# Kernel optimization log

Hardware: AMD Instinct MI355X
Metric: run time of the kernel (lower is better)

The kernel has to match this reference:

```python
import jax, jax.numpy as jnp
import numpy as np

D = 1024
H = 16
FF = 4096
B = 2
L = 2048
EPS = 1e-5


def setup_inputs() -> dict:
    key = jax.random.key(0)
    ks = jax.random.split(key, 12)
    s = 0.02
    return {
        "x": jax.random.normal(ks[0], (B, L, D), dtype=jnp.float32),
        "ln1_g": jnp.ones((D,), jnp.float32),
        "ln1_b": jnp.zeros((D,), jnp.float32),
        "qkv_w": jax.random.normal(ks[1], (D, 3 * D), dtype=jnp.float32) * s,
        "proj_w": jax.random.normal(ks[2], (D, D), dtype=jnp.float32) * s,
        "proj_b": jnp.zeros((D,), jnp.float32),
        "ln2_g": jnp.ones((D,), jnp.float32),
        "ln2_b": jnp.zeros((D,), jnp.float32),
        "w1": jax.random.normal(ks[3], (D, FF), dtype=jnp.float32) * s,
        "b1": jnp.zeros((FF,), jnp.float32),
        "w2": jax.random.normal(ks[4], (FF, D), dtype=jnp.float32) * s,
        "b2": jnp.zeros((D,), jnp.float32),
    }


def _layernorm(x, g, b):
    mu = jnp.mean(x, axis=-1, keepdims=True)
    var = jnp.var(x, axis=-1, keepdims=True)
    return (x - mu) * jax.lax.rsqrt(var + EPS) * g + b


def _attn(x, qkv_w, proj_w, proj_b):
    Bv, Lv, Dv = x.shape
    dk = Dv // H
    qkv = x @ qkv_w  # [B,L,3D]
    q, k, v = jnp.split(qkv, 3, axis=-1)

    def split(t):
        return t.reshape(Bv, Lv, H, dk).transpose(0, 2, 1, 3)  # [B,H,L,dk]

    q, k, v = map(split, (q, k, v))
    scores = jnp.einsum("bhqd,bhkd->bhqk", q, k) / np.sqrt(dk)
    attn = jax.nn.softmax(scores, axis=-1)
    out = jnp.einsum("bhqk,bhkd->bhqd", attn, v)
    out = out.transpose(0, 2, 1, 3).reshape(Bv, Lv, Dv)
    return out @ proj_w + proj_b


def reference(x, ln1_g, ln1_b, qkv_w, proj_w, proj_b, ln2_g, ln2_b, w1, b1, w2, b2):
    x = x + _attn(_layernorm(x, ln1_g, ln1_b), qkv_w, proj_w, proj_b)
    h = _layernorm(x, ln2_g, ln2_b)
    h = jax.nn.gelu(h @ w1 + b1, approximate=False) @ w2 + b2
    return x + h
```

## Files before the change

### kernel.cpp

```cpp
#include <hip/hip_runtime.h>
#include <cstdint>
#include <cstddef>

typedef __attribute__((ext_vector_type(8))) short bf16x8;
typedef __attribute__((ext_vector_type(4))) short bf16x4;
typedef __attribute__((ext_vector_type(4))) float f32x4;

__device__ __forceinline__ uint16_t f2bf(float f) {
    uint32_t u = __float_as_uint(f);
    u += 0x7FFFu + ((u >> 16) & 1u);
    return (uint16_t)(u >> 16);
}
__device__ __forceinline__ uint32_t bfr(float f) {
    return (__float_as_uint(f) + 0x8000u) >> 16;
}

__device__ __forceinline__ f32x4 mfma16(bf16x8 a, bf16x8 b, f32x4 c) {
    return __builtin_amdgcn_mfma_f32_16x16x32_bf16(a, b, c, 0, 0, 0);
}

__device__ __forceinline__ void async_copy16(const void* g, void* l) {
    __builtin_amdgcn_global_load_lds(
        (__attribute__((address_space(1))) void*)g,
        (__attribute__((address_space(3))) void*)l, 16, 0, 0);
}

typedef __attribute__((address_space(3))) const uint16_t lds_cu16;
__device__ __forceinline__ bf16x4 tr_read(lds_cu16* p) {
    bf16x4 d;
    asm volatile("ds_read_b64_tr_b16 %0, %1" : "=v"(d) : "v"(p));
    return d;
}
__device__ __forceinline__ bf16x8 cat8(bf16x4 lo, bf16x4 hi) {
    return __builtin_shufflevector(lo, hi, 0, 1, 2, 3, 4, 5, 6, 7);
}

__global__ __launch_bounds__(256) void transpose_cast(const float* __restrict__ W,
                                                      uint16_t* __restrict__ Wt,
                                                      int K, int N) {
    __shared__ uint16_t tile[32][33];
    const int n0 = blockIdx.x * 32, k0 = blockIdx.y * 32;
    const int tx = threadIdx.x, ty = threadIdx.y;
#pragma unroll
    for (int j = 0; j < 4; ++j) {
        int k = k0 + ty + j * 8;
        tile[ty + j * 8][tx] = f2bf(W[(size_t)k * N + n0 + tx]);
    }
    __syncthreads();
#pragma unroll
    for (int j = 0; j < 4; ++j) {
        int n = n0 + ty + j * 8;
        Wt[(size_t)n * K + k0 + tx] = tile[tx][ty + j * 8];
    }
}

__global__ __launch_bounds__(256) void ln_kernel(const float* __restrict__ x,
                                                 const float* __restrict__ g,
                                                 const float* __restrict__ b,
                                                 uint16_t* __restrict__ out) {
    const int row = blockIdx.x;
    const int t = threadIdx.x;
    const float* xr = x + (size_t)row * 1024;
    float4 v = *(const float4*)(xr + t * 4);
    float s = v.x + v.y + v.z + v.w;
    float s2 = v.x * v.x + v.y * v.y + v.z * v.z + v.w * v.w;
#pragma unroll
    for (int off = 1; off < 64; off <<= 1) {
        s += __shfl_xor(s, off);
        s2 += __shfl_xor(s2, off);
    }
    __shared__ float sh[8];
    const int wv = t >> 6;
    if ((t & 63) == 0) { sh[wv] = s; sh[4 + wv] = s2; }
    __syncthreads();
    s = sh[0] + sh[1] + sh[2] + sh[3];
    s2 = sh[4] + sh[5] + sh[6] + sh[7];
    const float mu = s * (1.f / 1024.f);
    const float var = s2 * (1.f / 1024.f) - mu * mu;
    const float rs = rsqrtf(var + 1e-5f);
    float4 gg = *(const float4*)(g + t * 4);
    float4 bb = *(const float4*)(b + t * 4);
    ushort4 ov;
    ov.x = f2bf((v.x - mu) * rs * gg.x + bb.x);
    ov.y = f2bf((v.y - mu) * rs * gg.y + bb.y);
    ov.z = f2bf((v.z - mu) * rs * gg.z + bb.z);
    ov.w = f2bf((v.w - mu) * rs * gg.w + bb.w);
    *(ushort4*)(out + (size_t)row * 1024 + t * 4) = ov;
}

template <int EPI, int BM, int BN>
__global__ __launch_bounds__(256) void gemm_bt(const uint16_t* __restrict__ A,
                                               const uint16_t* __restrict__ Bt,
                                               const float* __restrict__ bias,
                                               const float* __restrict__ resid,
                                               void* __restrict__ outp,
                                               int M, int N, int K) {
    __shared__ uint16_t As[BM * 64];
    __shared__ uint16_t Bs[BN * 64];
    const int t = threadIdx.x, lane = t & 63, w = t >> 6;
    const int l16 = lane & 15, lhi = lane >> 4;
    const int wr = w >> 1, wc = w & 1;
    const int m0 = blockIdx.x * BM, n0 = blockIdx.y * BN;
    constexpr int MI = BM / 32, NI = BN / 32;

    f32x4 acc[MI][NI];
    const f32x4 z = {0.f, 0.f, 0.f, 0.f};
#pragma unroll
    for (int mi = 0; mi < MI; ++mi)
#pragma unroll
        for (int ni = 0; ni < NI; ++ni) acc[mi][ni] = z;

    const int srow = lane >> 3;
    const int sgs = ((lane & 7) ^ srow) << 3;
    const uint16_t* Abase = A + (size_t)m0 * K;
    const uint16_t* Bbase = Bt + (size_t)n0 * K;

    for (int kt = 0; kt < K; kt += 64) {
        __syncthreads();
#pragma unroll
        for (int p = 0; p < BM / 32; ++p) {
            int r0 = w * (BM / 4) + p * 8;
            async_copy16(Abase + (size_t)(r0 + srow) * K + kt + sgs, &As[r0 * 64]);
        }
#pragma unroll
        for (int p = 0; p < BN / 32; ++p) {
            int r0 = w * (BN / 4) + p * 8;
            async_copy16(Bbase + (size_t)(r0 + srow) * K + kt + sgs, &Bs[r0 * 64]);
        }
        __syncthreads();
#pragma unroll
        for (int kh = 0; kh < 2; ++kh) {
            const int gk = kh * 4 + lhi;
            const int gsw = (gk ^ (l16 & 7)) << 3;
            bf16x8 af[MI], bfr[NI];
#pragma unroll
            for (int mi = 0; mi < MI; ++mi) {
                int rr = wr * (BM / 2) + mi * 16 + l16;
                af[mi] = *(const bf16x8*)&As[rr * 64 + gsw];
            }
#pragma unroll
            for (int ni = 0; ni < NI; ++ni) {
                int rr = wc * (BN / 2) + ni * 16 + l16;
                bfr[ni] = *(const bf16x8*)&Bs[rr * 64 + gsw];
            }
#pragma unroll
            for (int mi = 0; mi < MI; ++mi)
#pragma unroll
                for (int ni = 0; ni < NI; ++ni)
                    acc[mi][ni] = mfma16(af[mi], bfr[ni], acc[mi][ni]);
        }
    }

#pragma unroll
    for (int mi = 0; mi < MI; ++mi) {
#pragma unroll
        for (int ni = 0; ni < NI; ++ni) {
#pragma unroll
            for (int e = 0; e < 4; ++e) {
                int gm = m0 + wr * (BM / 2) + mi * 16 + 4 * lhi + e;
                int gn = n0 + wc * (BN / 2) + ni * 16 + l16;
                float v = acc[mi][ni][e];
                if constexpr (EPI == 0) {
                    ((uint16_t*)outp)[(size_t)gm * N + gn] = f2bf(v);
                } else if constexpr (EPI == 1) {
                    v += bias[gn] + resid[(size_t)gm * N + gn];
                    ((float*)outp)[(size_t)gm * N + gn] = v;
                } else {
                    v += bias[gn];
                    float gl = 0.5f * v * (1.f + erff(v * 0.70710678118f));
                    ((uint16_t*)outp)[(size_t)gm * N + gn] = f2bf(gl);
                }
            }
        }
    }
}

__global__ __launch_bounds__(256) void attn_kernel(const uint16_t* __restrict__ qkv,
                                                   uint16_t* __restrict__ aout) {
    __shared__ uint16_t Kt[2][64 * 64];
    __shared__ uint16_t Vs[2][64 * 64];
    __shared__ uint16_t Pt[4][64 * 16];
    const int qt = blockIdx.x, h = blockIdx.y, b = blockIdx.z;
    const int t = threadIdx.x, lane = t & 63, w = t >> 6;
    const int l16 = lane & 15, lhi = lane >> 4;
    const int q0 = qt * 64;
    const uint16_t* base = qkv + (size_t)(b * 2048) * 3072 + h * 64;

    bf16x8 aq[2];
    {
        const uint16_t* qp = base + (size_t)(q0 + w * 16 + l16) * 3072;
        aq[0] = *(const bf16x8*)(qp + 8 * lhi);
        aq[1] = *(const bf16x8*)(qp + 32 + 8 * lhi);
    }

    const int krow = lane >> 3;
    const int kgs = ((lane & 7) ^ krow) << 3;
    const int vkk = ((lane >> 5) << 2) | ((lane >> 1) & 3);
    const int vd  = (((lane >> 3) & 3) << 4) | ((lane & 1) << 3);

    auto stage = [&](int tile, int bufi) {
        const uint16_t* kb = base + (size_t)(tile * 64) * 3072 + 1024;
        const uint16_t* vb = base + (size_t)(tile * 64) * 3072 + 2048;
#pragma unroll
        for (int p = 0; p < 2; ++p) {
            int r0 = w * 16 + p * 8;
            async_copy16(kb + (size_t)(r0 + krow) * 3072 + kgs, &Kt[bufi][r0 * 64]);
        }
#pragma unroll
        for (int p = 0; p < 2; ++p) {
            int i = w * 2 + p;
            async_copy16(vb + (size_t)(i * 8 + vkk) * 3072 + vd, &Vs[bufi][i * 512]);
        }
    };

    const f32x4 z = {0.f, 0.f, 0.f, 0.f};
    f32x4 oacc[4];
#pragma unroll
    for (int n = 0; n < 4; ++n) oacc[n] = z;
    float mrun[4], lrun[4];
#pragma unroll
    for (int e = 0; e < 4; ++e) { mrun[e] = -1e30f; lrun[e] = 0.f; }
    const float cs = 0.18033688f;

    stage(0, 0);
    __syncthreads();

    for (int tile = 0; tile < 32; ++tile) {
        const int cur = tile & 1;
        if (tile + 1 < 32) stage(tile + 1, cur ^ 1);

        f32x4 sacc[4];
#pragma unroll
        for (int n = 0; n < 4; ++n) sacc[n] = z;
#pragma unroll
        for (int n = 0; n < 4; ++n) {
#pragma unroll
            for (int kh = 0; kh < 2; ++kh) {
                const int gk = kh * 4 + lhi;
                const int rr = n * 16 + l16;
                bf16x8 bk = *(const bf16x8*)&Kt[cur][rr * 64 + ((gk ^ (l16 & 7)) << 3)];
                sacc[n] = mfma16(aq[kh], bk, sacc[n]);
            }
        }

        float pv[4][4];
#pragma unroll
        for (int e = 0; e < 4; ++e) {
            float mx = fmaxf(fmaxf(sacc[0][e], sacc[1][e]), fmaxf(sacc[2][e], sacc[3][e]));
            mx = fmaxf(mx, __shfl_xor(mx, 1));
            mx = fmaxf(mx, __shfl_xor(mx, 2));
            mx = fmaxf(mx, __shfl_xor(mx, 4));
            mx = fmaxf(mx, __shfl_xor(mx, 8));
            const float mnew = fmaxf(mrun[e], mx);
            const float alpha = exp2f((mrun[e] - mnew) * cs);
            mrun[e] = mnew;
            const float mc = mnew * cs;
            float ps = 0.f;
#pragma unroll
            for (int n = 0; n < 4; ++n) {
                float p = exp2f(__fmaf_rn(sacc[n][e], cs, -mc));
                pv[n][e] = p;
                ps += p;
            }
            ps += __shfl_xor(ps, 1);
            ps += __shfl_xor(ps, 2);
            ps += __shfl_xor(ps, 4);
            ps += __shfl_xor(ps, 8);
            lrun[e] = lrun[e] * alpha + ps;
#pragma unroll
            for (int n = 0; n < 4; ++n) oacc[n][e] *= alpha;
        }

#pragma unroll
        for (int n = 0; n < 4; ++n) {
            uint2 pk;
            pk.x = bfr(pv[n][0]) | (bfr(pv[n][1]) << 16);
            pk.y = bfr(pv[n][2]) | (bfr(pv[n][3]) << 16);
            *(uint2*)&Pt[w][((n * 16 + l16) << 4) + (lhi << 2)] = pk;
        }
        asm volatile("s_waitcnt lgkmcnt(0)" ::: "memory");
        __builtin_amdgcn_sched_barrier(0);

        lds_cu16* ptb = (lds_cu16*)&Pt[w][0];
        lds_cu16* vtb = (lds_cu16*)&Vs[cur][0];
        bf16x8 pa[2], bv[4][2];
#pragma unroll
        for (int kh = 0; kh < 2; ++kh) {
            const int gk = kh * 4 + lhi;
            bf16x4 lo = tr_read(ptb + (gk << 7) + l16);
            bf16x4 hi = tr_read(ptb + (gk << 7) + 64 + l16);
            pa[kh] = cat8(lo, hi);
        }
#pragma unroll
        for (int n = 0; n < 4; ++n) {
#pragma unroll
            for (int kh = 0; kh < 2; ++kh) {
                const int gk = kh * 4 + lhi;
                bf16x4 lo = tr_read(vtb + ((gk * 2) << 8) + (n << 6) + l16);
                bf16x4 hi = tr_read(vtb + ((gk * 2 + 1) << 8) + (n << 6) + l16);
                bv[n][kh] = cat8(lo, hi);
            }
        }
        asm volatile("s_waitcnt lgkmcnt(0)" ::: "memory");
        __builtin_amdgcn_sched_barrier(0);

#pragma unroll
        for (int n = 0; n < 4; ++n)
#pragma unroll
            for (int kh = 0; kh < 2; ++kh)
                oacc[n] = mfma16(pa[kh], bv[n][kh], oacc[n]);

        __syncthreads();
    }

#pragma unroll
    for (int n = 0; n < 4; ++n) {
#pragma unroll
        for (int e = 0; e < 4; ++e) {
            int qrow = q0 + w * 16 + 4 * lhi + e;
            float v = oacc[n][e] / lrun[e];
            aout[(size_t)(b * 2048 + qrow) * 1024 + h * 64 + n * 16 + l16] = f2bf(v);
        }
    }
}

extern "C" void kernel_launch(void* const* d_in, const int* in_sizes, int n_in,
                              void* d_out, int out_size, void* d_ws, size_t ws_size,
                              hipStream_t stream) {
    const float* x      = (const float*)d_in[0];
    const float* ln1_g  = (const float*)d_in[1];
    const float* ln1_b  = (const float*)d_in[2];
    const float* qkv_w  = (const float*)d_in[3];
    const float* proj_w = (const float*)d_in[4];
    const float* proj_b = (const float*)d_in[5];
    const float* ln2_g  = (const float*)d_in[6];
    const float* ln2_b  = (const float*)d_in[7];
    const float* w1     = (const float*)d_in[8];
    const float* b1     = (const float*)d_in[9];
    const float* w2     = (const float*)d_in[10];
    const float* b2     = (const float*)d_in[11];
    float* out = (float*)d_out;

    char* ws = (char*)d_ws;
    size_t off = 0;
    auto alloc = [&](size_t bytes) {
        void* p = ws + off;
        off += (bytes + 255) & ~(size_t)255;
        return p;
    };
    uint16_t* wqkv_t  = (uint16_t*)alloc((size_t)3072 * 1024 * 2);
    uint16_t* wproj_t = (uint16_t*)alloc((size_t)1024 * 1024 * 2);
    uint16_t* w1_t    = (uint16_t*)alloc((size_t)4096 * 1024 * 2);
    uint16_t* w2_t    = (uint16_t*)alloc((size_t)1024 * 4096 * 2);
    float*    x2      = (float*)   alloc((size_t)4096 * 1024 * 4);
    uint16_t* lnb     = (uint16_t*)alloc((size_t)4096 * 1024 * 2);
    uint16_t* qkvb    = (uint16_t*)alloc((size_t)4096 * 3072 * 2);
    uint16_t* attnb   = (uint16_t*)alloc((size_t)4096 * 1024 * 2);
    uint16_t* h1      = qkvb;

    dim3 tb(32, 8, 1);
    transpose_cast<<<dim3(3072 / 32, 1024 / 32), tb, 0, stream>>>(qkv_w, wqkv_t, 1024, 3072);
    transpose_cast<<<dim3(1024 / 32, 1024 / 32), tb, 0, stream>>>(proj_w, wproj_t, 1024, 1024);
    transpose_cast<<<dim3(4096 / 32, 1024 / 32), tb, 0, stream>>>(w1, w1_t, 1024, 4096);
    transpose_cast<<<dim3(1024 / 32, 4096 / 32), tb, 0, stream>>>(w2, w2_t, 4096, 1024);

    ln_kernel<<<4096, 256, 0, stream>>>(x, ln1_g, ln1_b, lnb);
    gemm_bt<0, 128, 128><<<dim3(32, 24), 256, 0, stream>>>(lnb, wqkv_t, nullptr, nullptr, qkvb, 4096, 3072, 1024);
    attn_kernel<<<dim3(32, 16, 2), 256, 0, stream>>>(qkvb, attnb);
    gemm_bt<1, 64, 128><<<dim3(64, 8), 256, 0, stream>>>(attnb, wproj_t, proj_b, x, x2, 4096, 1024, 1024);
    ln_kernel<<<4096, 256, 0, stream>>>(x2, ln2_g, ln2_b, lnb);
    gemm_bt<2, 128, 128><<<dim3(32, 32), 256, 0, stream>>>(lnb, w1_t, b1, nullptr, h1, 4096, 4096, 1024);
    gemm_bt<1, 64, 128><<<dim3(64, 8), 256, 0, stream>>>(h1, w2_t, b2, x2, out, 4096, 1024, 4096);
}
```

Measured before the change: 332.9 us.

## Transpose attention MFMA layout so each lane owns a query row, add lazy rescale

Swaps the MFMA operand order so S^T and O^T are computed, which puts one query row per lane column. Row max and sum then need only two cross-lane shuffles instead of four per element, and the softmax state becomes one scalar per lane. The running max is only updated when it grows by more than a threshold, skipping the output rescale otherwise. P is now stored row-major with an XOR swizzle and read back with plain vector loads instead of transposed reads, and the output is written as vectorized 4-element stores. The skipped rescale relies on the bounded exponent staying within float range.

```diff
diff --git a/kernel.cpp b/kernel.cpp
--- a/kernel.cpp
+++ b/kernel.cpp
@@ -179,7 +179,7 @@
                                                    uint16_t* __restrict__ aout) {
     __shared__ uint16_t Kt[2][64 * 64];
     __shared__ uint16_t Vs[2][64 * 64];
-    __shared__ uint16_t Pt[4][64 * 16];
+    __shared__ uint16_t Pq[4][16 * 64];
     const int qt = blockIdx.x, h = blockIdx.y, b = blockIdx.z;
     const int t = threadIdx.x, lane = t & 63, w = t >> 6;
     const int l16 = lane & 15, lhi = lane >> 4;
@@ -214,12 +214,10 @@
     };
 
     const f32x4 z = {0.f, 0.f, 0.f, 0.f};
-    f32x4 oacc[4];
-#pragma unroll
-    for (int n = 0; n < 4; ++n) oacc[n] = z;
-    float mrun[4], lrun[4];
-#pragma unroll
-    for (int e = 0; e < 4; ++e) { mrun[e] = -1e30f; lrun[e] = 0.f; }
+    f32x4 oaccT[4];
+#pragma unroll
+    for (int n = 0; n < 4; ++n) oaccT[n] = z;
+    float mrun = -1e30f, lrun = 0.f;
     const float cs = 0.18033688f;
 
     stage(0, 0);
@@ -231,66 +229,74 @@
 
         f32x4 sacc[4];
 #pragma unroll
-        for (int n = 0; n < 4; ++n) sacc[n] = z;
-#pragma unroll
-        for (int n = 0; n < 4; ++n) {
+        for (int nk = 0; nk < 4; ++nk) sacc[nk] = z;
+#pragma unroll
+        for (int nk = 0; nk < 4; ++nk) {
 #pragma unroll
             for (int kh = 0; kh < 2; ++kh) {
                 const int gk = kh * 4 + lhi;
-                const int rr = n * 16 + l16;
+                const int rr = nk * 16 + l16;
                 bf16x8 bk = *(const bf16x8*)&Kt[cur][rr * 64 + ((gk ^ (l16 & 7)) << 3)];
-                sacc[n] = mfma16(aq[kh], bk, sacc[n]);
-            }
-        }
-
-        float pv[4][4];
-#pragma unroll
-        for (int e = 0; e < 4; ++e) {
-            float mx = fmaxf(fmaxf(sacc[0][e], sacc[1][e]), fmaxf(sacc[2][e], sacc[3][e]));
-            mx = fmaxf(mx, __shfl_xor(mx, 1));
-            mx = fmaxf(mx, __shfl_xor(mx, 2));
-            mx = fmaxf(mx, __shfl_xor(mx, 4));
-            mx = fmaxf(mx, __shfl_xor(mx, 8));
-            const float mnew = fmaxf(mrun[e], mx);
-            const float alpha = exp2f((mrun[e] - mnew) * cs);
-            mrun[e] = mnew;
-            const float mc = mnew * cs;
-            float ps = 0.f;
-#pragma unroll
-            for (int n = 0; n < 4; ++n) {
-                float p = exp2f(__fmaf_rn(sacc[n][e], cs, -mc));
-                pv[n][e] = p;
-                ps += p;
-            }
-            ps += __shfl_xor(ps, 1);
-            ps += __shfl_xor(ps, 2);
-            ps += __shfl_xor(ps, 4);
-            ps += __shfl_xor(ps, 8);
-            lrun[e] = lrun[e] * alpha + ps;
-#pragma unroll
-            for (int n = 0; n < 4; ++n) oacc[n][e] *= alpha;
-        }
-
-#pragma unroll
-        for (int n = 0; n < 4; ++n) {
+                sacc[nk] = mfma16(bk, aq[kh], sacc[nk]);
+            }
+        }
+
+        float mx = -1e30f;
+#pragma unroll
+        for (int nk = 0; nk < 4; ++nk)
+#pragma unroll
+            for (int e = 0; e < 4; ++e) mx = fmaxf(mx, sacc[nk][e]);
+        mx = fmaxf(mx, __shfl_xor(mx, 16));
+        mx = fmaxf(mx, __shfl_xor(mx, 32));
+
+        const bool keep = __all(mx - mrun <= 44.0f);
+        float alpha = 1.f;
+        if (!keep) {
+            float mnew = fmaxf(mrun, mx);
+            alpha = exp2f((mrun - mnew) * cs);
+            mrun = mnew;
+        }
+        const float mc = mrun * cs;
+
+        float p[4][4];
+        float ps = 0.f;
+#pragma unroll
+        for (int nk = 0; nk < 4; ++nk)
+#pragma unroll
+            for (int e = 0; e < 4; ++e) {
+                float pe = exp2f(__fmaf_rn(sacc[nk][e], cs, -mc));
+                p[nk][e] = pe;
+                ps += pe;
+            }
+        ps += __shfl_xor(ps, 16);
+        ps += __shfl_xor(ps, 32);
+        if (!keep) {
+            lrun = lrun * alpha + ps;
+#pragma unroll
+            for (int n = 0; n < 4; ++n) oaccT[n] *= alpha;
+        } else {
+            lrun += ps;
+        }
+
+#pragma unroll
+        for (int nk = 0; nk < 4; ++nk) {
             uint2 pk;
-            pk.x = bfr(pv[n][0]) | (bfr(pv[n][1]) << 16);
-            pk.y = bfr(pv[n][2]) | (bfr(pv[n][3]) << 16);
-            *(uint2*)&Pt[w][((n * 16 + l16) << 4) + (lhi << 2)] = pk;
+            pk.x = bfr(p[nk][0]) | (bfr(p[nk][1]) << 16);
+            pk.y = bfr(p[nk][2]) | (bfr(p[nk][3]) << 16);
+            const int g = nk * 2 + (lhi >> 1);
+            *(uint2*)&Pq[w][l16 * 64 + ((g ^ (l16 & 7)) << 3) + ((lhi & 1) << 2)] = pk;
         }
         asm volatile("s_waitcnt lgkmcnt(0)" ::: "memory");
         __builtin_amdgcn_sched_barrier(0);
 
-        lds_cu16* ptb = (lds_cu16*)&Pt[w][0];
-        lds_cu16* vtb = (lds_cu16*)&Vs[cur][0];
-        bf16x8 pa[2], bv[4][2];
+        bf16x8 pa[2];
 #pragma unroll
         for (int kh = 0; kh < 2; ++kh) {
             const int gk = kh * 4 + lhi;
-            bf16x4 lo = tr_read(ptb + (gk << 7) + l16);
-            bf16x4 hi = tr_read(ptb + (gk << 7) + 64 + l16);
-            pa[kh] = cat8(lo, hi);
-        }
+            pa[kh] = *(const bf16x8*)&Pq[w][l16 * 64 + ((gk ^ (l16 & 7)) << 3)];
+        }
+        lds_cu16* vtb = (lds_cu16*)&Vs[cur][0];
+        bf16x8 bv[4][2];
 #pragma unroll
         for (int n = 0; n < 4; ++n) {
 #pragma unroll
@@ -308,19 +314,21 @@
         for (int n = 0; n < 4; ++n)
 #pragma unroll
             for (int kh = 0; kh < 2; ++kh)
-                oacc[n] = mfma16(pa[kh], bv[n][kh], oacc[n]);
+                oaccT[n] = mfma16(bv[n][kh], pa[kh], oaccT[n]);
 
         __syncthreads();
     }
 
+    const float rl = 1.0f / lrun;
+    const size_t orow = (size_t)(b * 2048 + q0 + w * 16 + l16) * 1024 + h * 64;
 #pragma unroll
     for (int n = 0; n < 4; ++n) {
-#pragma unroll
-        for (int e = 0; e < 4; ++e) {
-            int qrow = q0 + w * 16 + 4 * lhi + e;
-            float v = oacc[n][e] / lrun[e];
-            aout[(size_t)(b * 2048 + qrow) * 1024 + h * 64 + n * 16 + l16] = f2bf(v);
-        }
+        ushort4 ov;
+        ov.x = f2bf(oaccT[n][0] * rl);
+        ov.y = f2bf(oaccT[n][1] * rl);
+        ov.z = f2bf(oaccT[n][2] * rl);
+        ov.w = f2bf(oaccT[n][3] * rl);
+        *(ushort4*)&aout[orow + n * 16 + 4 * lhi] = ov;
     }
 }
 
```

New measurement: 274.5 us. 17.5% less time.
